# Kernel tuning notes

Hardware: AMD Instinct MI355X
Metric: run time of the kernel (lower is better)

Reference implementation:

```python
import jax, jax.numpy as jnp
import numpy as np

# dims: batch, seq, d_model, d_hidden, routed experts, top-k, shared experts
B, S, D, H, E_R, K, E_S = 2, 1024, 1024, 512, 64, 6, 2
EPS = 1.1920929e-07  # torch.finfo(float32).eps, RMSNorm default when eps=None


def setup_inputs() -> dict:
    key = jax.random.key(0)
    ks = jax.random.split(key, 8)
    u = lambda k, shape, b: jax.random.uniform(k, shape, jnp.float32, -b, b)
    bd = 1.0 / np.sqrt(D)   # bound for W1 (1/sqrt(d_input)) and W2 (1/sqrt(d_output)=1/sqrt(D))
    bh = 1.0 / np.sqrt(H)
    return {
        "x": jax.random.normal(ks[0], (B, S, D), jnp.float32),
        "norm_w": jnp.ones((D,), jnp.float32),            # RMSNorm weight
        "Wr": u(ks[1], (E_R, D), bd),                      # router Linear weight (no bias)
        "sW1": u(ks[2], (E_S, D, H), bd), "sb1": jnp.zeros((E_S, 1, H), jnp.float32),
        "sW2": u(ks[3], (E_S, H, D), bd), "sb2": jnp.zeros((E_S, 1, D), jnp.float32),
        "sWg": u(ks[4], (H, H), bh),                       # shared-experts SwiGLU gate weight
        "rW1": u(ks[5], (E_R, D, H), bd), "rb1": jnp.zeros((E_R, 1, H), jnp.float32),
        "rW2": u(ks[6], (E_R, H, D), bd), "rb2": jnp.zeros((E_R, 1, D), jnp.float32),
        "rWg": u(ks[7], (H, H), bh),                       # routed-experts SwiGLU gate weight
        "bias": jnp.full((E_R,), 1.0 / E_R, jnp.float32), # routing bias buffer (expert_bias=True)
    }


def _rmsnorm(x, w):
    ms = jnp.mean(x * x, axis=-1, keepdims=True)
    return x * jax.lax.rsqrt(ms + EPS) * w


def _swiglu(h, Wg):
    # SwiGLU(d_model=H): silu(h @ Wg) * h, elementwise gate over hidden dim
    return jax.nn.silu(h @ Wg) * h


def reference(x, norm_w, Wr, sW1, sb1, sW2, sb2, sWg, rW1, rb1, rW2, rb2, rWg, bias):
    xn = _rmsnorm(x, norm_w)
    t = xn.reshape(-1, D)                                  # (T, D) tokens
    # --- shared experts, summed over expert axis ---
    hs = jnp.einsum('td,edh->teh', t, sW1) + sb1[None, :, 0, :]
    hs = _swiglu(hs, sWg)
    shared = jnp.einsum('teh,ehd->td', hs, sW2) + jnp.sum(sb2[:, 0, :], axis=0)
    # --- router ---
    raw = t @ Wr.T                                         # (T, E_R) raw affinity
    aff = jax.lax.stop_gradient(raw) + bias                # detached + bias for top-k selection
    _, idx = jax.lax.top_k(aff, K)                         # (T, K)
    # --- routed experts: dense all-expert FFN, gather top-k outputs ---
    # (mathematically identical to the source's per-token weight gather,
    #  but avoids materializing (T,K,D,H) weight tensors)
    h = jnp.einsum('td,edh->teh', t, rW1) + rb1[None, :, 0, :]   # (T, E_R, H)
    h = _swiglu(h, rWg)
    out_all = jnp.einsum('teh,ehd->ted', h, rW2) + rb2[None, :, 0, :]  # (T, E_R, D)
    out_k = jnp.take_along_axis(out_all, idx[:, :, None], axis=1)      # (T, K, D)
    aff_k = jnp.take_along_axis(raw, idx, axis=1)                      # (T, K) raw (undetached)
    w = aff_k / jnp.sum(aff_k, axis=-1, keepdims=True)                 # expert_bias=True path
    routed = jnp.einsum('tk,tkd->td', w, out_k)                        # (T, D)
    return x + (shared + routed).reshape(B, S, D)
```

## Files before the change

### kernel.cpp

```cpp
#include <hip/hip_runtime.h>
#include <cstdint>
#include <cstddef>

typedef unsigned short u16;
typedef unsigned int u32;
typedef __attribute__((ext_vector_type(8))) short bh8;
typedef __attribute__((ext_vector_type(4))) float fx4;

#define T_TOK 2048
#define D_DIM 1024
#define H_DIM 512
#define N_EXP 64
#define K_TOP 6
#define N_ASG (T_TOK * K_TOP)

__device__ __forceinline__ float bf2f(u16 v) {
    union { u32 u; float f; } c; c.u = ((u32)v) << 16; return c.f;
}
__device__ __forceinline__ u16 f2bf(float f) {
    union { u32 u; float f; } c; c.f = f;
    u32 u = c.u;
    return (u16)((u + 0x7fffu + ((u >> 16) & 1u)) >> 16);
}

__global__ __launch_bounds__(256) void routernorm_k(
    const float* __restrict__ x, const float* __restrict__ nw,
    const float* __restrict__ Wr, float* __restrict__ raw, u16* __restrict__ xnb)
{
    int t = blockIdx.x, tid = threadIdx.x;
    __shared__ float xs[D_DIM];
    __shared__ float ps[256];
    __shared__ float red[4];
    int d0 = tid << 2;
    float4 xv = *(const float4*)(x + (size_t)t * D_DIM + d0);
    float ss = xv.x * xv.x + xv.y * xv.y + xv.z * xv.z + xv.w * xv.w;
    #pragma unroll
    for (int o = 32; o > 0; o >>= 1) ss += __shfl_down(ss, o);
    if ((tid & 63) == 0) red[tid >> 6] = ss;
    __syncthreads();
    float ms = (red[0] + red[1] + red[2] + red[3]) * (1.f / (float)D_DIM);
    float sc = rsqrtf(ms + 1.1920929e-07f);
    float4 wv = *(const float4*)(nw + d0);
    float4 xf;
    xf.x = xv.x * sc * wv.x;
    xf.y = xv.y * sc * wv.y;
    xf.z = xv.z * sc * wv.z;
    xf.w = xv.w * sc * wv.w;
    *(float4*)&xs[d0] = xf;
    ushort4 ob;
    ob.x = f2bf(xf.x); ob.y = f2bf(xf.y); ob.z = f2bf(xf.z); ob.w = f2bf(xf.w);
    *(ushort4*)(xnb + (size_t)t * D_DIM + d0) = ob;
    __syncthreads();
    int e = tid & 63, part = tid >> 6;
    const float* wr = Wr + (size_t)e * D_DIM + part * 256;
    const float* xp = &xs[part * 256];
    float s = 0.f;
    #pragma unroll 8
    for (int i = 0; i < 256; i += 4) {
        float4 w4 = *(const float4*)(wr + i);
        s += xp[i] * w4.x + xp[i + 1] * w4.y + xp[i + 2] * w4.z + xp[i + 3] * w4.w;
    }
    ps[tid] = s;
    __syncthreads();
    if (part == 0) raw[(size_t)t * N_EXP + e] = ps[e] + ps[64 + e] + ps[128 + e] + ps[192 + e];
}

__global__ void topk_k(const float* __restrict__ raw, const float* __restrict__ ebias,
                       int* __restrict__ cnt, int* __restrict__ tki, float* __restrict__ tkw)
{
    int t = blockIdx.x, lane = threadIdx.x;
    float r = raw[(size_t)t * N_EXP + lane];
    float cur = r + ebias[lane];
    int selI[K_TOP]; float selR[K_TOP];
    #pragma unroll
    for (int k = 0; k < K_TOP; ++k) {
        float v = cur; int id = lane;
        #pragma unroll
        for (int o = 32; o > 0; o >>= 1) {
            float v2 = __shfl_down(v, o); int i2 = __shfl_down(id, o);
            if (v2 > v || (v2 == v && i2 < id)) { v = v2; id = i2; }
        }
        id = __shfl(id, 0);
        if (lane == id) cur = -3.4e38f;
        selI[k] = id;
        selR[k] = __shfl(r, id);
    }
    float s = 0.f;
    #pragma unroll
    for (int k = 0; k < K_TOP; ++k) s += selR[k];
    if (lane < K_TOP) {
        tki[t * K_TOP + lane] = selI[lane];
        tkw[t * K_TOP + lane] = selR[lane] / s;
        atomicAdd(&cnt[selI[lane]], 1);
    }
}

__global__ void scan_k(const int* __restrict__ cnt, int* __restrict__ offs, int* __restrict__ fill)
{
    int lane = threadIdx.x;
    int c = cnt[lane];
    int s = c;
    #pragma unroll
    for (int o = 1; o < 64; o <<= 1) {
        int v = __shfl_up(s, o);
        if (lane >= o) s += v;
    }
    int excl = s - c;
    offs[lane] = excl;
    fill[lane] = excl;
    if (lane == 63) offs[N_EXP] = s;
}

__global__ void fill_k(const int* __restrict__ tki, const float* __restrict__ tkw,
                       int* __restrict__ fill, int* __restrict__ atok, float* __restrict__ aw)
{
    int t = blockIdx.x, lane = threadIdx.x;
    if (lane < K_TOP) {
        int e = tki[t * K_TOP + lane];
        int p = atomicAdd(&fill[e], 1);
        atok[p] = t;
        aw[p] = tkw[t * K_TOP + lane];
    }
}

__global__ __launch_bounds__(256) void convAll_k(
    const float* __restrict__ rW1, const float* __restrict__ sW1,
    const float* __restrict__ rW2, const float* __restrict__ sW2,
    const float* __restrict__ rWg, const float* __restrict__ sWg,
    u16* __restrict__ W1f, u16* __restrict__ W2f, u16* __restrict__ Wgf)
{
    int id = blockIdx.x;
    const float* src; u16* dst;
    int K, N, n0, k0;
    const size_t MS = (size_t)H_DIM * D_DIM;
    if (id < 66 * 128) {
        int mat = id >> 7, tile = id & 127;
        K = D_DIM; N = H_DIM;
        src = (mat < N_EXP ? rW1 + (size_t)mat * MS : sW1 + (size_t)(mat - N_EXP) * MS);
        dst = W1f + (size_t)mat * MS;
        n0 = (tile & 7) << 6; k0 = (tile >> 3) << 6;
    } else if (id < 2 * 66 * 128) {
        id -= 66 * 128;
        int mat = id >> 7, tile = id & 127;
        K = H_DIM; N = D_DIM;
        src = (mat < N_EXP ? rW2 + (size_t)mat * MS : sW2 + (size_t)(mat - N_EXP) * MS);
        dst = W2f + (size_t)mat * MS;
        n0 = (tile & 15) << 6; k0 = (tile >> 4) << 6;
    } else {
        id -= 2 * 66 * 128;
        int mat = id >> 6, tile = id & 63;
        K = H_DIM; N = H_DIM;
        src = (mat == 0 ? rWg : sWg);
        dst = Wgf + (size_t)mat * (H_DIM * H_DIM);
        n0 = (tile & 7) << 6; k0 = (tile >> 3) << 6;
    }

    __shared__ u16 t[64][72];
    int tid = threadIdx.x;
    int kr = tid >> 4, c4 = (tid & 15) << 2;
    #pragma unroll
    for (int rr = 0; rr < 4; ++rr) {
        int k = (rr << 4) + kr;
        float4 v = *(const float4*)(src + (size_t)(k0 + k) * N + n0 + c4);
        t[c4 + 0][k] = f2bf(v.x);
        t[c4 + 1][k] = f2bf(v.y);
        t[c4 + 2][k] = f2bf(v.z);
        t[c4 + 3][k] = f2bf(v.w);
    }
    __syncthreads();
    int lane = tid & 63, g = tid >> 6;
    int nr = lane & 15, kq = lane >> 4;
    #pragma unroll
    for (int f = 0; f < 2; ++f) {
        int fragId = g + (f << 2);
        int ntile = fragId >> 1, kb = fragId & 1;
        bh8 v = *(const bh8*)&t[(ntile << 4) + nr][(kb << 5) + (kq << 3)];
        size_t fi = (((size_t)((n0 >> 4) + ntile) * (size_t)(K >> 5)
                      + (size_t)((k0 >> 5) + kb)) << 9) + (size_t)(lane << 3);
        *(bh8*)(dst + fi) = v;
    }
}

__global__ __launch_bounds__(256, 2) void moe_ffn6_k(
    const u16* __restrict__ xnb,
    const u16* __restrict__ W1f,
    const u16* __restrict__ Wgf,
    const u16* __restrict__ W2f,
    const float* __restrict__ rb1, const float* __restrict__ rb2,
    const float* __restrict__ sb1, const float* __restrict__ sb2,
    const int* __restrict__ offs, const int* __restrict__ atok,
    const float* __restrict__ aw, float* __restrict__ accG)
{
    int id = blockIdx.x;
    int xcd = id & 7, rest = id >> 3, grp = rest >> 6, slab = rest & 63;
    int e, rowBase, end;
    bool routed;
    if (grp < 8) {
        e = (grp << 3) + xcd;
        routed = true;
        rowBase = offs[e] + (slab << 5);
        end = offs[e + 1];
    } else {
        int f = (slab << 3) + xcd;
        if (f >= 128) return;
        e = N_EXP + (f & 1);
        routed = false;
        rowBase = (f >> 1) << 5;
        end = T_TOK;
    }
    if (rowBase >= end) return;
    int rows = end - rowBase; if (rows > 32) rows = 32;

    __shared__ int   tok[32];
    __shared__ float wt[32];
    __shared__ u16 hA[32 * 520];

    int tid = threadIdx.x;
    if (tid < 32) {
        int cl = rowBase + tid; if (cl >= end) cl = end - 1;
        tok[tid] = routed ? atok[cl] : cl;
        wt[tid]  = routed ? aw[cl] : 1.0f;
    }
    __syncthreads();

    int w = tid >> 6, lane = tid & 63, quad = lane >> 4, l15 = lane & 15;
    int n0w = w << 7;

    const u16* W1e = W1f + (size_t)e * (H_DIM * D_DIM);
    const u16* W2e = W2f + (size_t)e * (H_DIM * D_DIM);
    const u16* Wge = Wgf + (routed ? 0 : (size_t)(H_DIM * H_DIM));
    const float* b1 = routed ? rb1 + e * H_DIM : sb1 + (e - N_EXP) * H_DIM;
    const float* b2 = routed ? rb2 + e * D_DIM : sb2 + (e - N_EXP) * D_DIM;

    {
        const u16* a0p = xnb + (size_t)tok[l15] * D_DIM + (quad << 3);
        const u16* a1p = xnb + (size_t)tok[16 + l15] * D_DIM + (quad << 3);
        const u16* bp  = W1e + ((size_t)w << 17) + (lane << 3);
        fx4 ac0[8] = {}, ac1[8] = {};
        bh8 bA[8], bB[8], aA0, aA1, aB0, aB1;
        #pragma unroll
        for (int ct = 0; ct < 8; ++ct) bA[ct] = *(const bh8*)(bp + (ct << 14));
        aA0 = *(const bh8*)a0p;
        aA1 = *(const bh8*)a1p;
        #pragma unroll 1
        for (int kbi = 0; kbi < 32; kbi += 2) {
            #pragma unroll
            for (int ct = 0; ct < 8; ++ct) bB[ct] = *(const bh8*)(bp + (((ct << 5) + kbi + 1) << 9));
            aB0 = *(const bh8*)(a0p + ((kbi + 1) << 5));
            aB1 = *(const bh8*)(a1p + ((kbi + 1) << 5));
            #pragma unroll
            for (int ct = 0; ct < 8; ++ct) {
                ac0[ct] = __builtin_amdgcn_mfma_f32_16x16x32_bf16(aA0, bA[ct], ac0[ct], 0, 0, 0);
                ac1[ct] = __builtin_amdgcn_mfma_f32_16x16x32_bf16(aA1, bA[ct], ac1[ct], 0, 0, 0);
            }
            #pragma unroll
            for (int ct = 0; ct < 8; ++ct) bA[ct] = *(const bh8*)(bp + (((ct << 5) + kbi + 2) << 9));
            aA0 = *(const bh8*)(a0p + ((kbi + 2) << 5));
            aA1 = *(const bh8*)(a1p + ((kbi + 2) << 5));
            #pragma unroll
            for (int ct = 0; ct < 8; ++ct) {
                ac0[ct] = __builtin_amdgcn_mfma_f32_16x16x32_bf16(aB0, bB[ct], ac0[ct], 0, 0, 0);
                ac1[ct] = __builtin_amdgcn_mfma_f32_16x16x32_bf16(aB1, bB[ct], ac1[ct], 0, 0, 0);
            }
        }
        #pragma unroll
        for (int ct = 0; ct < 8; ++ct) {
            int col = n0w + (ct << 4) + l15;
            float bv = b1[col];
            #pragma unroll
            for (int r = 0; r < 4; ++r) {
                int r0 = (quad << 2) + r;
                hA[r0 * 520 + col]        = f2bf(ac0[ct][r] + bv);
                hA[(16 + r0) * 520 + col] = f2bf(ac1[ct][r] + bv);
            }
        }
    }
    __syncthreads();

    {
        const u16* A0 = hA + l15 * 520 + (quad << 3);
        const u16* A1 = hA + (16 + l15) * 520 + (quad << 3);
        const u16* bp = Wge + ((size_t)w << 16) + (lane << 3);
        fx4 ac0[8] = {}, ac1[8] = {};
        bh8 bA[8], bB[8], aA0, aA1, aB0, aB1;
        #pragma unroll
        for (int ct = 0; ct < 8; ++ct) bA[ct] = *(const bh8*)(bp + (ct << 13));
        aA0 = *(const bh8*)A0;
        aA1 = *(const bh8*)A1;
        #pragma unroll 1
        for (int kbi = 0; kbi < 16; kbi += 2) {
            #pragma unroll
            for (int ct = 0; ct < 8; ++ct) bB[ct] = *(const bh8*)(bp + (((ct << 4) + kbi + 1) << 9));
            aB0 = *(const bh8*)(A0 + ((kbi + 1) << 5));
            aB1 = *(const bh8*)(A1 + ((kbi + 1) << 5));
            #pragma unroll
            for (int ct = 0; ct < 8; ++ct) {
                ac0[ct] = __builtin_amdgcn_mfma_f32_16x16x32_bf16(aA0, bA[ct], ac0[ct], 0, 0, 0);
                ac1[ct] = __builtin_amdgcn_mfma_f32_16x16x32_bf16(aA1, bA[ct], ac1[ct], 0, 0, 0);
            }
            #pragma unroll
            for (int ct = 0; ct < 8; ++ct) bA[ct] = *(const bh8*)(bp + (((ct << 4) + kbi + 2) << 9));
            aA0 = *(const bh8*)(A0 + ((kbi + 2) << 5));
            aA1 = *(const bh8*)(A1 + ((kbi + 2) << 5));
            #pragma unroll
            for (int ct = 0; ct < 8; ++ct) {
                ac0[ct] = __builtin_amdgcn_mfma_f32_16x16x32_bf16(aB0, bB[ct], ac0[ct], 0, 0, 0);
                ac1[ct] = __builtin_amdgcn_mfma_f32_16x16x32_bf16(aB1, bB[ct], ac1[ct], 0, 0, 0);
            }
        }
        __syncthreads();
        #pragma unroll
        for (int ct = 0; ct < 8; ++ct) {
            int col = n0w + (ct << 4) + l15;
            #pragma unroll
            for (int r = 0; r < 4; ++r) {
                int r0 = (quad << 2) + r;
                float g0 = ac0[ct][r];
                float h0 = bf2f(hA[r0 * 520 + col]);
                hA[r0 * 520 + col] = f2bf(h0 * g0 * (1.f / (1.f + __expf(-g0))));
                int r1 = 16 + r0;
                float g1 = ac1[ct][r];
                float h1 = bf2f(hA[r1 * 520 + col]);
                hA[r1 * 520 + col] = f2bf(h1 * g1 * (1.f / (1.f + __expf(-g1))));
            }
        }
    }
    __syncthreads();

    #pragma unroll 1
    for (int half = 0; half < 2; ++half) {
        int n0 = (w << 8) + (half << 7);
        const u16* A0 = hA + l15 * 520 + (quad << 3);
        const u16* A1 = hA + (16 + l15) * 520 + (quad << 3);
        const u16* bp = W2e + (((size_t)((w << 4) + (half << 3))) << 13) + (lane << 3);
        fx4 ac0[8] = {}, ac1[8] = {};
        bh8 bA[8], bB[8], aA0, aA1, aB0, aB1;
        #pragma unroll
        for (int ct = 0; ct < 8; ++ct) bA[ct] = *(const bh8*)(bp + (ct << 13));
        aA0 = *(const bh8*)A0;
        aA1 = *(const bh8*)A1;
        #pragma unroll 1
        for (int kbi = 0; kbi < 16; kbi += 2) {
            #pragma unroll
            for (int ct = 0; ct < 8; ++ct) bB[ct] = *(const bh8*)(bp + (((ct << 4) + kbi + 1) << 9));
            aB0 = *(const bh8*)(A0 + ((kbi + 1) << 5));
            aB1 = *(const bh8*)(A1 + ((kbi + 1) << 5));
            #pragma unroll
            for (int ct = 0; ct < 8; ++ct) {
                ac0[ct] = __builtin_amdgcn_mfma_f32_16x16x32_bf16(aA0, bA[ct], ac0[ct], 0, 0, 0);
                ac1[ct] = __builtin_amdgcn_mfma_f32_16x16x32_bf16(aA1, bA[ct], ac1[ct], 0, 0, 0);
            }
            #pragma unroll
            for (int ct = 0; ct < 8; ++ct) bA[ct] = *(const bh8*)(bp + (((ct << 4) + kbi + 2) << 9));
            aA0 = *(const bh8*)(A0 + ((kbi + 2) << 5));
            aA1 = *(const bh8*)(A1 + ((kbi + 2) << 5));
            #pragma unroll
            for (int ct = 0; ct < 8; ++ct) {
                ac0[ct] = __builtin_amdgcn_mfma_f32_16x16x32_bf16(aB0, bB[ct], ac0[ct], 0, 0, 0);
                ac1[ct] = __builtin_amdgcn_mfma_f32_16x16x32_bf16(aB1, bB[ct], ac1[ct], 0, 0, 0);
            }
        }
        #pragma unroll
        for (int ct = 0; ct < 8; ++ct) {
            int col = n0 + (ct << 4) + l15;
            float bv = b2[col];
            #pragma unroll
            for (int r = 0; r < 4; ++r) {
                int r0 = (quad << 2) + r;
                if (r0 < rows)
                    atomicAdd(&accG[(size_t)tok[r0] * D_DIM + col], wt[r0] * (ac0[ct][r] + bv));
                int r1 = 16 + r0;
                if (r1 < rows)
                    atomicAdd(&accG[(size_t)tok[r1] * D_DIM + col], wt[r1] * (ac1[ct][r] + bv));
            }
        }
    }
}

template<int ROUTED>
__global__ __launch_bounds__(256) void moe_ffn_k(
    const u16* __restrict__ xnb,
    const float* __restrict__ W1b, const float* __restrict__ Wg,
    const float* __restrict__ W2b,
    const float* __restrict__ b1b, const float* __restrict__ b2b,
    const int* __restrict__ offs, const int* __restrict__ atok,
    const float* __restrict__ aw, float* __restrict__ accG)
{
    int e = blockIdx.z;
    int start = ROUTED ? offs[e] : 0;
    int end   = ROUTED ? offs[e + 1] : T_TOK;
    int rowBase = start + (blockIdx.y << 5);
    if (rowBase >= end) return;
    int rows = end - rowBase; if (rows > 32) rows = 32;

    __shared__ int   tok[32];
    __shared__ float wt[32];
    __shared__ u16 hA[32 * 520];
    __shared__ u16 hG[32 * 520];
    __shared__ u16 As[32 * 32];
    __shared__ u16 Bs[64 * 36];

    int tid = threadIdx.x;
    if (tid < 32) {
        int cl = rowBase + tid; if (cl >= end) cl = end - 1;
        tok[tid] = ROUTED ? atok[cl] : cl;
        wt[tid]  = ROUTED ? aw[cl] : 1.0f;
    }
    __syncthreads();

    const float* W1 = W1b + (size_t)e * (D_DIM * H_DIM);
    const float* W2 = W2b + (size_t)e * (D_DIM * H_DIM);
    const float* b1 = b1b + e * H_DIM;
    const float* b2 = b2b + e * D_DIM;

    int w = tid >> 6, lane = tid & 63, quad = lane >> 4, l15 = lane & 15;
    int sr2 = tid >> 3, sc2 = (tid & 7) << 2;

    for (int nc = 0; nc < 8; ++nc) {
        int n0 = nc << 6;
        fx4 a0 = {}; fx4 a1 = {};
        for (int kc = 0; kc < 32; ++kc) {
            int kb = kc << 5;
            int2 av = *(const int2*)(xnb + (size_t)tok[sr2] * D_DIM + kb + sc2);
            const float* cp = W1 + n0 + lane;
            int kx = kb + (w << 3);
            u32 p[4];
            #pragma unroll
            for (int jj = 0; jj < 4; ++jj) {
                u32 lo = f2bf(cp[(size_t)(kx + 2 * jj) * H_DIM]);
                u32 hi = f2bf(cp[(size_t)(kx + 2 * jj + 1) * H_DIM]);
                p[jj] = lo | (hi << 16);
            }
            __syncthreads();
            *(int2*)&As[sr2 * 32 + sc2] = av;
            u16* bsw = &Bs[lane * 36 + (w << 3)];
            uint2 q0; q0.x = p[0]; q0.y = p[1];
            uint2 q1; q1.x = p[2]; q1.y = p[3];
            *(uint2*)bsw = q0;
            *(uint2*)(bsw + 4) = q1;
            __syncthreads();
            bh8 af0 = *(const bh8*)&As[l15 * 32 + (quad << 3)];
            bh8 af1 = *(const bh8*)&As[(16 + l15) * 32 + (quad << 3)];
            const u16* brp = &Bs[((w << 4) + l15) * 36 + (quad << 3)];
            union { bh8 v; uint2 u2[2]; } bf;
            bf.u2[0] = *(const uint2*)brp;
            bf.u2[1] = *(const uint2*)(brp + 4);
            a0 = __builtin_amdgcn_mfma_f32_16x16x32_bf16(af0, bf.v, a0, 0, 0, 0);
            a1 = __builtin_amdgcn_mfma_f32_16x16x32_bf16(af1, bf.v, a1, 0, 0, 0);
        }
        int col = n0 + (w << 4) + l15;
        float bv = b1[col];
        #pragma unroll
        for (int r = 0; r < 4; ++r) {
            hA[((quad << 2) + r) * 520 + col]      = f2bf(a0[r] + bv);
            hA[(16 + (quad << 2) + r) * 520 + col] = f2bf(a1[r] + bv);
        }
    }
    __syncthreads();

    for (int nc = 0; nc < 8; ++nc) {
        int n0 = nc << 6;
        fx4 a0 = {}; fx4 a1 = {};
        for (int kc = 0; kc < 16; ++kc) {
            int kb = kc << 5;
            const float* cp = Wg + n0 + lane;
            int kx = kb + (w << 3);
            u32 p[4];
            #pragma unroll
            for (int jj = 0; jj < 4; ++jj) {
                u32 lo = f2bf(cp[(size_t)(kx + 2 * jj) * H_DIM]);
                u32 hi = f2bf(cp[(size_t)(kx + 2 * jj + 1) * H_DIM]);
                p[jj] = lo | (hi << 16);
            }
            __syncthreads();
            u16* bsw = &Bs[lane * 36 + (w << 3)];
            uint2 q0; q0.x = p[0]; q0.y = p[1];
            uint2 q1; q1.x = p[2]; q1.y = p[3];
            *(uint2*)bsw = q0;
            *(uint2*)(bsw + 4) = q1;
            __syncthreads();
            bh8 af0 = *(const bh8*)&hA[l15 * 520 + kb + (quad << 3)];
            bh8 af1 = *(const bh8*)&hA[(16 + l15) * 520 + kb + (quad << 3)];
            const u16* brp = &Bs[((w << 4) + l15) * 36 + (quad << 3)];
            union { bh8 v; uint2 u2[2]; } bf;
            bf.u2[0] = *(const uint2*)brp;
            bf.u2[1] = *(const uint2*)(brp + 4);
            a0 = __builtin_amdgcn_mfma_f32_16x16x32_bf16(af0, bf.v, a0, 0, 0, 0);
            a1 = __builtin_amdgcn_mfma_f32_16x16x32_bf16(af1, bf.v, a1, 0, 0, 0);
        }
        int col = n0 + (w << 4) + l15;
        #pragma unroll
        for (int r = 0; r < 4; ++r) {
            int r0 = (quad << 2) + r;
            float h0 = bf2f(hA[r0 * 520 + col]);
            float g0 = a0[r];
            hG[r0 * 520 + col] = f2bf(h0 * g0 * (1.f / (1.f + __expf(-g0))));
            int r1 = 16 + r0;
            float h1 = bf2f(hA[r1 * 520 + col]);
            float g1 = a1[r];
            hG[r1 * 520 + col] = f2bf(h1 * g1 * (1.f / (1.f + __expf(-g1))));
        }
    }
    __syncthreads();

    for (int nc = 0; nc < 16; ++nc) {
        int n0 = nc << 6;
        fx4 a0 = {}; fx4 a1 = {};
        for (int kc = 0; kc < 16; ++kc) {
            int kb = kc << 5;
            const float* cp = W2 + n0 + lane;
            int kx = kb + (w << 3);
            u32 p[4];
            #pragma unroll
            for (int jj = 0; jj < 4; ++jj) {
                u32 lo = f2bf(cp[(size_t)(kx + 2 * jj) * D_DIM]);
                u32 hi = f2bf(cp[(size_t)(kx + 2 * jj + 1) * D_DIM]);
                p[jj] = lo | (hi << 16);
            }
            __syncthreads();
            u16* bsw = &Bs[lane * 36 + (w << 3)];
            uint2 q0; q0.x = p[0]; q0.y = p[1];
            uint2 q1; q1.x = p[2]; q1.y = p[3];
            *(uint2*)bsw = q0;
            *(uint2*)(bsw + 4) = q1;
            __syncthreads();
            bh8 af0 = *(const bh8*)&hG[l15 * 520 + kb + (quad << 3)];
            bh8 af1 = *(const bh8*)&hG[(16 + l15) * 520 + kb + (quad << 3)];
            const u16* brp = &Bs[((w << 4) + l15) * 36 + (quad << 3)];
            union { bh8 v; uint2 u2[2]; } bf;
            bf.u2[0] = *(const uint2*)brp;
            bf.u2[1] = *(const uint2*)(brp + 4);
            a0 = __builtin_amdgcn_mfma_f32_16x16x32_bf16(af0, bf.v, a0, 0, 0, 0);
            a1 = __builtin_amdgcn_mfma_f32_16x16x32_bf16(af1, bf.v, a1, 0, 0, 0);
        }
        int col = n0 + (w << 4) + l15;
        float bv = b2[col];
        #pragma unroll
        for (int r = 0; r < 4; ++r) {
            int lr0 = (quad << 2) + r;
            if (lr0 < rows)
                atomicAdd(&accG[(size_t)tok[lr0] * D_DIM + col], wt[lr0] * (a0[r] + bv));
            int lr1 = 16 + lr0;
            if (lr1 < rows)
                atomicAdd(&accG[(size_t)tok[lr1] * D_DIM + col], wt[lr1] * (a1[r] + bv));
        }
    }
}

__global__ __launch_bounds__(256) void final_k(
    const float* __restrict__ x, const float* __restrict__ acc, float* __restrict__ out)
{
    size_t i = ((size_t)blockIdx.x * 256 + threadIdx.x) << 2;
    float4 xv = *(const float4*)(x + i);
    float4 a = *(const float4*)(acc + i);
    float4 o;
    o.x = xv.x + a.x;
    o.y = xv.y + a.y;
    o.z = xv.z + a.z;
    o.w = xv.w + a.w;
    *(float4*)(out + i) = o;
}

extern "C" void kernel_launch(void* const* d_in, const int* in_sizes, int n_in,
                              void* d_out, int out_size, void* d_ws, size_t ws_size,
                              hipStream_t stream)
{
    const float* x     = (const float*)d_in[0];
    const float* nw    = (const float*)d_in[1];
    const float* Wr    = (const float*)d_in[2];
    const float* sW1   = (const float*)d_in[3];
    const float* sb1   = (const float*)d_in[4];
    const float* sW2   = (const float*)d_in[5];
    const float* sb2   = (const float*)d_in[6];
    const float* sWg   = (const float*)d_in[7];
    const float* rW1   = (const float*)d_in[8];
    const float* rb1   = (const float*)d_in[9];
    const float* rW2   = (const float*)d_in[10];
    const float* rb2   = (const float*)d_in[11];
    const float* rWg   = (const float*)d_in[12];
    const float* ebias = (const float*)d_in[13];
    float* out = (float*)d_out;
    (void)in_sizes; (void)n_in; (void)out_size;

    char* wp = (char*)d_ws;
    auto alloc = [&](size_t b) { char* p = wp; wp += (b + 255) & ~(size_t)255; return p; };
    int*   cnt  = (int*)alloc(N_EXP * 4);
    int*   offs = (int*)alloc((N_EXP + 1) * 4);
    int*   fill = (int*)alloc(N_EXP * 4);
    int*   tki  = (int*)alloc((size_t)T_TOK * K_TOP * 4);
    float* tkw  = (float*)alloc((size_t)T_TOK * K_TOP * 4);
    int*   atok = (int*)alloc((size_t)N_ASG * 4);
    float* aw   = (float*)alloc((size_t)N_ASG * 4);
    float* raw  = (float*)alloc((size_t)T_TOK * N_EXP * 4);
    u16*   xnb  = (u16*)alloc((size_t)T_TOK * D_DIM * 2);
    float* acc  = (float*)alloc((size_t)T_TOK * D_DIM * 4);
    u16* W1f = (u16*)alloc((size_t)(N_EXP + 2) * H_DIM * D_DIM * 2);
    u16* W2f = (u16*)alloc((size_t)(N_EXP + 2) * H_DIM * D_DIM * 2);
    u16* Wgf = (u16*)alloc((size_t)2 * H_DIM * H_DIM * 2);
    alloc(1 << 16);
    bool fast = (size_t)(wp - (char*)d_ws) <= ws_size;

    hipMemsetAsync(cnt, 0, N_EXP * 4, stream);
    hipMemsetAsync(acc, 0, (size_t)T_TOK * D_DIM * 4, stream);

    dim3 b256(256);
    routernorm_k<<<T_TOK, b256, 0, stream>>>(x, nw, Wr, raw, xnb);
    topk_k<<<T_TOK, dim3(64), 0, stream>>>(raw, ebias, cnt, tki, tkw);
    scan_k<<<1, dim3(64), 0, stream>>>(cnt, offs, fill);
    fill_k<<<T_TOK, dim3(64), 0, stream>>>(tki, tkw, fill, atok, aw);

    if (fast) {
        convAll_k<<<dim3(2 * 66 * 128 + 2 * 64), b256, 0, stream>>>(
            rW1, sW1, rW2, sW2, rWg, sWg, W1f, W2f, Wgf);

        moe_ffn6_k<<<dim3(8 * 9 * 64), b256, 0, stream>>>(
            xnb, W1f, Wgf, W2f, rb1, rb2, sb1, sb2, offs, atok, aw, acc);
    } else {
        moe_ffn_k<1><<<dim3(1, 64, N_EXP), b256, 0, stream>>>(
            xnb, rW1, rWg, rW2, rb1, rb2, offs, atok, aw, acc);
        moe_ffn_k<0><<<dim3(1, 64, 2), b256, 0, stream>>>(
            xnb, sW1, sWg, sW2, sb1, sb2, offs, atok, aw, acc);
    }

    final_k<<<(T_TOK * D_DIM) / 1024, b256, 0, stream>>>(x, acc, out);
}
```

Baseline: 716.6 us.

## Split fused expert FFN into three GEMM kernels and batch router-norm tokens

The single fused expert kernel, which computed W1, the SwiGLU gate and W2 per 32-row slab using shared memory, is replaced by three separate kernels. They exchange intermediate hidden activations through global bf16 buffers, and each kernel splits the output columns over an extra grid dimension. This gives many more, lighter blocks with higher occupancy hints, aiming to improve latency hiding and load balance. The cost is extra global memory traffic for the intermediate buffers and two more launches. The router/RMSNorm kernel also now handles 4 tokens per block, so each router weight load is reused across those tokens.

```diff
diff --git a/kernel.cpp b/kernel.cpp
--- a/kernel.cpp
+++ b/kernel.cpp
@@ -13,6 +13,8 @@
 #define N_EXP 64
 #define K_TOP 6
 #define N_ASG (T_TOK * K_TOP)
+#define R_TOT (N_ASG + 2 * T_TOK)
+#define GRID_E (8 * 9 * 64)
 
 __device__ __forceinline__ float bf2f(u16 v) {
     union { u32 u; float f; } c; c.u = ((u32)v) << 16; return c.f;
@@ -23,46 +25,65 @@
     return (u16)((u + 0x7fffu + ((u >> 16) & 1u)) >> 16);
 }
 
-__global__ __launch_bounds__(256) void routernorm_k(
+__global__ __launch_bounds__(256) void rn4_k(
     const float* __restrict__ x, const float* __restrict__ nw,
     const float* __restrict__ Wr, float* __restrict__ raw, u16* __restrict__ xnb)
 {
-    int t = blockIdx.x, tid = threadIdx.x;
-    __shared__ float xs[D_DIM];
-    __shared__ float ps[256];
-    __shared__ float red[4];
+    int t0 = blockIdx.x << 2, tid = threadIdx.x;
+    __shared__ float xs[4][D_DIM];
+    __shared__ float ps[4][256];
+    __shared__ float red4[4][4];
     int d0 = tid << 2;
-    float4 xv = *(const float4*)(x + (size_t)t * D_DIM + d0);
-    float ss = xv.x * xv.x + xv.y * xv.y + xv.z * xv.z + xv.w * xv.w;
-    #pragma unroll
-    for (int o = 32; o > 0; o >>= 1) ss += __shfl_down(ss, o);
-    if ((tid & 63) == 0) red[tid >> 6] = ss;
-    __syncthreads();
-    float ms = (red[0] + red[1] + red[2] + red[3]) * (1.f / (float)D_DIM);
-    float sc = rsqrtf(ms + 1.1920929e-07f);
     float4 wv = *(const float4*)(nw + d0);
-    float4 xf;
-    xf.x = xv.x * sc * wv.x;
-    xf.y = xv.y * sc * wv.y;
-    xf.z = xv.z * sc * wv.z;
-    xf.w = xv.w * sc * wv.w;
-    *(float4*)&xs[d0] = xf;
-    ushort4 ob;
-    ob.x = f2bf(xf.x); ob.y = f2bf(xf.y); ob.z = f2bf(xf.z); ob.w = f2bf(xf.w);
-    *(ushort4*)(xnb + (size_t)t * D_DIM + d0) = ob;
+    float4 xv[4];
+    #pragma unroll
+    for (int tt = 0; tt < 4; ++tt) {
+        xv[tt] = *(const float4*)(x + (size_t)(t0 + tt) * D_DIM + d0);
+        float ss = xv[tt].x * xv[tt].x + xv[tt].y * xv[tt].y
+                 + xv[tt].z * xv[tt].z + xv[tt].w * xv[tt].w;
+        #pragma unroll
+        for (int o = 32; o > 0; o >>= 1) ss += __shfl_down(ss, o);
+        if ((tid & 63) == 0) red4[tt][tid >> 6] = ss;
+    }
+    __syncthreads();
+    #pragma unroll
+    for (int tt = 0; tt < 4; ++tt) {
+        float ms = (red4[tt][0] + red4[tt][1] + red4[tt][2] + red4[tt][3]) * (1.f / (float)D_DIM);
+        float sc = rsqrtf(ms + 1.1920929e-07f);
+        float4 xf;
+        xf.x = xv[tt].x * sc * wv.x;
+        xf.y = xv[tt].y * sc * wv.y;
+        xf.z = xv[tt].z * sc * wv.z;
+        xf.w = xv[tt].w * sc * wv.w;
+        *(float4*)&xs[tt][d0] = xf;
+        ushort4 ob;
+        ob.x = f2bf(xf.x); ob.y = f2bf(xf.y); ob.z = f2bf(xf.z); ob.w = f2bf(xf.w);
+        *(ushort4*)(xnb + (size_t)(t0 + tt) * D_DIM + d0) = ob;
+    }
     __syncthreads();
     int e = tid & 63, part = tid >> 6;
     const float* wr = Wr + (size_t)e * D_DIM + part * 256;
-    const float* xp = &xs[part * 256];
-    float s = 0.f;
-    #pragma unroll 8
+    float s0 = 0.f, s1 = 0.f, s2 = 0.f, s3 = 0.f;
+    const float* xp0 = &xs[0][part * 256];
+    const float* xp1 = &xs[1][part * 256];
+    const float* xp2 = &xs[2][part * 256];
+    const float* xp3 = &xs[3][part * 256];
+    #pragma unroll 4
     for (int i = 0; i < 256; i += 4) {
         float4 w4 = *(const float4*)(wr + i);
-        s += xp[i] * w4.x + xp[i + 1] * w4.y + xp[i + 2] * w4.z + xp[i + 3] * w4.w;
-    }
-    ps[tid] = s;
-    __syncthreads();
-    if (part == 0) raw[(size_t)t * N_EXP + e] = ps[e] + ps[64 + e] + ps[128 + e] + ps[192 + e];
+        s0 += xp0[i] * w4.x + xp0[i+1] * w4.y + xp0[i+2] * w4.z + xp0[i+3] * w4.w;
+        s1 += xp1[i] * w4.x + xp1[i+1] * w4.y + xp1[i+2] * w4.z + xp1[i+3] * w4.w;
+        s2 += xp2[i] * w4.x + xp2[i+1] * w4.y + xp2[i+2] * w4.z + xp2[i+3] * w4.w;
+        s3 += xp3[i] * w4.x + xp3[i+1] * w4.y + xp3[i+2] * w4.z + xp3[i+3] * w4.w;
+    }
+    ps[0][tid] = s0; ps[1][tid] = s1; ps[2][tid] = s2; ps[3][tid] = s3;
+    __syncthreads();
+    if (part == 0) {
+        #pragma unroll
+        for (int tt = 0; tt < 4; ++tt)
+            raw[(size_t)(t0 + tt) * N_EXP + e] =
+                ps[tt][e] + ps[tt][64 + e] + ps[tt][128 + e] + ps[tt][192 + e];
+    }
 }
 
 __global__ void topk_k(const float* __restrict__ raw, const float* __restrict__ ebias,
@@ -181,198 +202,218 @@
     }
 }
 
-__global__ __launch_bounds__(256, 2) void moe_ffn6_k(
-    const u16* __restrict__ xnb,
-    const u16* __restrict__ W1f,
-    const u16* __restrict__ Wgf,
-    const u16* __restrict__ W2f,
-    const float* __restrict__ rb1, const float* __restrict__ rb2,
-    const float* __restrict__ sb1, const float* __restrict__ sb2,
+__device__ __forceinline__ bool slabDecode(
+    int bx, const int* __restrict__ offs,
+    int& e, int& rowBase, int& rows, int& tokBase)
+{
+    int xcd = bx & 7, rest = bx >> 3, grp = rest >> 6, slab = rest & 63;
+    if (grp < 8) {
+        e = (grp << 3) + xcd;
+        int s0 = offs[e], s1 = offs[e + 1];
+        rowBase = s0 + (slab << 5);
+        if (rowBase >= s1) return false;
+        rows = s1 - rowBase; if (rows > 32) rows = 32;
+        tokBase = -1;
+        return true;
+    }
+    int f = (slab << 3) + xcd;
+    if (f >= 128) return false;
+    int sh = f & 1;
+    e = N_EXP + sh;
+    tokBase = (f >> 1) << 5;
+    rowBase = N_ASG + (sh << 11) + tokBase;
+    rows = 32;
+    return true;
+}
+
+__global__ __launch_bounds__(256, 4) void p1_k(
+    const u16* __restrict__ xnb, const u16* __restrict__ W1f,
+    const float* __restrict__ rb1, const float* __restrict__ sb1,
+    const int* __restrict__ offs, const int* __restrict__ atok,
+    u16* __restrict__ h)
+{
+    int e, rowBase, rows, tokBase;
+    if (!slabDecode(blockIdx.x, offs, e, rowBase, rows, tokBase)) return;
+
+    __shared__ int tok[32];
+    int tid = threadIdx.x;
+    if (tid < 32) {
+        int cl = tid < rows ? tid : rows - 1;
+        tok[tid] = (tokBase < 0) ? atok[rowBase + cl] : tokBase + tid;
+    }
+    __syncthreads();
+
+    int w = tid >> 6, lane = tid & 63, quad = lane >> 4, l15 = lane & 15;
+    int cg = blockIdx.y;
+    int nt0 = (cg << 4) + (w << 2);
+    const u16* bp = W1f + (size_t)e * (H_DIM * D_DIM)
+                  + (((size_t)nt0 << 5) << 9) + (lane << 3);
+    const u16* a0p = xnb + (size_t)tok[l15] * D_DIM + (quad << 3);
+    const u16* a1p = xnb + (size_t)tok[16 + l15] * D_DIM + (quad << 3);
+    const float* b1 = (tokBase < 0) ? rb1 + e * H_DIM : sb1 + (e - N_EXP) * H_DIM;
+
+    fx4 ac0[4] = {}, ac1[4] = {};
+    bh8 bA[4], bB[4], aA0, aA1, aB0, aB1;
+    #pragma unroll
+    for (int ct = 0; ct < 4; ++ct) bA[ct] = *(const bh8*)(bp + ((size_t)(ct << 5) << 9));
+    aA0 = *(const bh8*)a0p; aA1 = *(const bh8*)a1p;
+    #pragma unroll 1
+    for (int kb = 0; kb < 32; kb += 2) {
+        #pragma unroll
+        for (int ct = 0; ct < 4; ++ct) bB[ct] = *(const bh8*)(bp + (((ct << 5) + kb + 1) << 9));
+        aB0 = *(const bh8*)(a0p + ((kb + 1) << 5));
+        aB1 = *(const bh8*)(a1p + ((kb + 1) << 5));
+        #pragma unroll
+        for (int ct = 0; ct < 4; ++ct) {
+            ac0[ct] = __builtin_amdgcn_mfma_f32_16x16x32_bf16(aA0, bA[ct], ac0[ct], 0, 0, 0);
+            ac1[ct] = __builtin_amdgcn_mfma_f32_16x16x32_bf16(aA1, bA[ct], ac1[ct], 0, 0, 0);
+        }
+        #pragma unroll
+        for (int ct = 0; ct < 4; ++ct) bA[ct] = *(const bh8*)(bp + (((ct << 5) + kb + 2) << 9));
+        aA0 = *(const bh8*)(a0p + ((kb + 2) << 5));
+        aA1 = *(const bh8*)(a1p + ((kb + 2) << 5));
+        #pragma unroll
+        for (int ct = 0; ct < 4; ++ct) {
+            ac0[ct] = __builtin_amdgcn_mfma_f32_16x16x32_bf16(aB0, bB[ct], ac0[ct], 0, 0, 0);
+            ac1[ct] = __builtin_amdgcn_mfma_f32_16x16x32_bf16(aB1, bB[ct], ac1[ct], 0, 0, 0);
+        }
+    }
+    #pragma unroll
+    for (int ct = 0; ct < 4; ++ct) {
+        int col = ((nt0 + ct) << 4) + l15;
+        float bv = b1[col];
+        #pragma unroll
+        for (int r = 0; r < 4; ++r) {
+            int r0 = (quad << 2) + r;
+            if (r0 < rows) h[(size_t)(rowBase + r0) * H_DIM + col] = f2bf(ac0[ct][r] + bv);
+            int r1 = 16 + r0;
+            if (r1 < rows) h[(size_t)(rowBase + r1) * H_DIM + col] = f2bf(ac1[ct][r] + bv);
+        }
+    }
+}
+
+__global__ __launch_bounds__(256, 4) void p2_k(
+    const u16* __restrict__ hbuf, const u16* __restrict__ Wgf, u16* __restrict__ hg)
+{
+    int rowBase = blockIdx.x << 5;
+    int tid = threadIdx.x;
+    int w = tid >> 6, lane = tid & 63, quad = lane >> 4, l15 = lane & 15;
+    int cg = blockIdx.y;
+    int nt0 = (cg << 4) + (w << 2);
+    const u16* bp = Wgf + (rowBase < N_ASG ? 0 : (size_t)(H_DIM * H_DIM))
+                  + (((size_t)nt0 << 4) << 9) + (lane << 3);
+    const u16* a0p = hbuf + (size_t)(rowBase + l15) * H_DIM + (quad << 3);
+    const u16* a1p = hbuf + (size_t)(rowBase + 16 + l15) * H_DIM + (quad << 3);
+
+    fx4 ac0[4] = {}, ac1[4] = {};
+    bh8 bA[4], bB[4], aA0, aA1, aB0, aB1;
+    #pragma unroll
+    for (int ct = 0; ct < 4; ++ct) bA[ct] = *(const bh8*)(bp + ((size_t)(ct << 4) << 9));
+    aA0 = *(const bh8*)a0p; aA1 = *(const bh8*)a1p;
+    #pragma unroll 1
+    for (int kb = 0; kb < 16; kb += 2) {
+        #pragma unroll
+        for (int ct = 0; ct < 4; ++ct) bB[ct] = *(const bh8*)(bp + (((ct << 4) + kb + 1) << 9));
+        aB0 = *(const bh8*)(a0p + ((kb + 1) << 5));
+        aB1 = *(const bh8*)(a1p + ((kb + 1) << 5));
+        #pragma unroll
+        for (int ct = 0; ct < 4; ++ct) {
+            ac0[ct] = __builtin_amdgcn_mfma_f32_16x16x32_bf16(aA0, bA[ct], ac0[ct], 0, 0, 0);
+            ac1[ct] = __builtin_amdgcn_mfma_f32_16x16x32_bf16(aA1, bA[ct], ac1[ct], 0, 0, 0);
+        }
+        #pragma unroll
+        for (int ct = 0; ct < 4; ++ct) bA[ct] = *(const bh8*)(bp + (((ct << 4) + kb + 2) << 9));
+        aA0 = *(const bh8*)(a0p + ((kb + 2) << 5));
+        aA1 = *(const bh8*)(a1p + ((kb + 2) << 5));
+        #pragma unroll
+        for (int ct = 0; ct < 4; ++ct) {
+            ac0[ct] = __builtin_amdgcn_mfma_f32_16x16x32_bf16(aB0, bB[ct], ac0[ct], 0, 0, 0);
+            ac1[ct] = __builtin_amdgcn_mfma_f32_16x16x32_bf16(aB1, bB[ct], ac1[ct], 0, 0, 0);
+        }
+    }
+    #pragma unroll
+    for (int ct = 0; ct < 4; ++ct) {
+        int col = ((nt0 + ct) << 4) + l15;
+        #pragma unroll
+        for (int r = 0; r < 4; ++r) {
+            int r0 = (quad << 2) + r;
+            size_t i0 = (size_t)(rowBase + r0) * H_DIM + col;
+            float g0 = ac0[ct][r], h0 = bf2f(hbuf[i0]);
+            hg[i0] = f2bf(h0 * g0 * (1.f / (1.f + __expf(-g0))));
+            int r1 = 16 + r0;
+            size_t i1 = (size_t)(rowBase + r1) * H_DIM + col;
+            float g1 = ac1[ct][r], h1 = bf2f(hbuf[i1]);
+            hg[i1] = f2bf(h1 * g1 * (1.f / (1.f + __expf(-g1))));
+        }
+    }
+}
+
+__global__ __launch_bounds__(256, 4) void p3_k(
+    const u16* __restrict__ hg, const u16* __restrict__ W2f,
+    const float* __restrict__ rb2, const float* __restrict__ sb2,
     const int* __restrict__ offs, const int* __restrict__ atok,
     const float* __restrict__ aw, float* __restrict__ accG)
 {
-    int id = blockIdx.x;
-    int xcd = id & 7, rest = id >> 3, grp = rest >> 6, slab = rest & 63;
-    int e, rowBase, end;
-    bool routed;
-    if (grp < 8) {
-        e = (grp << 3) + xcd;
-        routed = true;
-        rowBase = offs[e] + (slab << 5);
-        end = offs[e + 1];
-    } else {
-        int f = (slab << 3) + xcd;
-        if (f >= 128) return;
-        e = N_EXP + (f & 1);
-        routed = false;
-        rowBase = (f >> 1) << 5;
-        end = T_TOK;
-    }
-    if (rowBase >= end) return;
-    int rows = end - rowBase; if (rows > 32) rows = 32;
-
-    __shared__ int   tok[32];
+    int e, rowBase, rows, tokBase;
+    if (!slabDecode(blockIdx.x, offs, e, rowBase, rows, tokBase)) return;
+
+    __shared__ int tok[32];
     __shared__ float wt[32];
-    __shared__ u16 hA[32 * 520];
-
     int tid = threadIdx.x;
     if (tid < 32) {
-        int cl = rowBase + tid; if (cl >= end) cl = end - 1;
-        tok[tid] = routed ? atok[cl] : cl;
-        wt[tid]  = routed ? aw[cl] : 1.0f;
+        int cl = tid < rows ? tid : rows - 1;
+        if (tokBase < 0) { tok[tid] = atok[rowBase + cl]; wt[tid] = aw[rowBase + cl]; }
+        else             { tok[tid] = tokBase + tid;      wt[tid] = 1.0f; }
     }
     __syncthreads();
 
     int w = tid >> 6, lane = tid & 63, quad = lane >> 4, l15 = lane & 15;
-    int n0w = w << 7;
-
-    const u16* W1e = W1f + (size_t)e * (H_DIM * D_DIM);
-    const u16* W2e = W2f + (size_t)e * (H_DIM * D_DIM);
-    const u16* Wge = Wgf + (routed ? 0 : (size_t)(H_DIM * H_DIM));
-    const float* b1 = routed ? rb1 + e * H_DIM : sb1 + (e - N_EXP) * H_DIM;
-    const float* b2 = routed ? rb2 + e * D_DIM : sb2 + (e - N_EXP) * D_DIM;
-
-    {
-        const u16* a0p = xnb + (size_t)tok[l15] * D_DIM + (quad << 3);
-        const u16* a1p = xnb + (size_t)tok[16 + l15] * D_DIM + (quad << 3);
-        const u16* bp  = W1e + ((size_t)w << 17) + (lane << 3);
-        fx4 ac0[8] = {}, ac1[8] = {};
-        bh8 bA[8], bB[8], aA0, aA1, aB0, aB1;
-        #pragma unroll
-        for (int ct = 0; ct < 8; ++ct) bA[ct] = *(const bh8*)(bp + (ct << 14));
-        aA0 = *(const bh8*)a0p;
-        aA1 = *(const bh8*)a1p;
-        #pragma unroll 1
-        for (int kbi = 0; kbi < 32; kbi += 2) {
-            #pragma unroll
-            for (int ct = 0; ct < 8; ++ct) bB[ct] = *(const bh8*)(bp + (((ct << 5) + kbi + 1) << 9));
-            aB0 = *(const bh8*)(a0p + ((kbi + 1) << 5));
-            aB1 = *(const bh8*)(a1p + ((kbi + 1) << 5));
-            #pragma unroll
-            for (int ct = 0; ct < 8; ++ct) {
-                ac0[ct] = __builtin_amdgcn_mfma_f32_16x16x32_bf16(aA0, bA[ct], ac0[ct], 0, 0, 0);
-                ac1[ct] = __builtin_amdgcn_mfma_f32_16x16x32_bf16(aA1, bA[ct], ac1[ct], 0, 0, 0);
-            }
-            #pragma unroll
-            for (int ct = 0; ct < 8; ++ct) bA[ct] = *(const bh8*)(bp + (((ct << 5) + kbi + 2) << 9));
-            aA0 = *(const bh8*)(a0p + ((kbi + 2) << 5));
-            aA1 = *(const bh8*)(a1p + ((kbi + 2) << 5));
-            #pragma unroll
-            for (int ct = 0; ct < 8; ++ct) {
-                ac0[ct] = __builtin_amdgcn_mfma_f32_16x16x32_bf16(aB0, bB[ct], ac0[ct], 0, 0, 0);
-                ac1[ct] = __builtin_amdgcn_mfma_f32_16x16x32_bf16(aB1, bB[ct], ac1[ct], 0, 0, 0);
-            }
-        }
-        #pragma unroll
-        for (int ct = 0; ct < 8; ++ct) {
-            int col = n0w + (ct << 4) + l15;
-            float bv = b1[col];
-            #pragma unroll
-            for (int r = 0; r < 4; ++r) {
-                int r0 = (quad << 2) + r;
-                hA[r0 * 520 + col]        = f2bf(ac0[ct][r] + bv);
-                hA[(16 + r0) * 520 + col] = f2bf(ac1[ct][r] + bv);
-            }
-        }
-    }
-    __syncthreads();
-
-    {
-        const u16* A0 = hA + l15 * 520 + (quad << 3);
-        const u16* A1 = hA + (16 + l15) * 520 + (quad << 3);
-        const u16* bp = Wge + ((size_t)w << 16) + (lane << 3);
-        fx4 ac0[8] = {}, ac1[8] = {};
-        bh8 bA[8], bB[8], aA0, aA1, aB0, aB1;
-        #pragma unroll
-        for (int ct = 0; ct < 8; ++ct) bA[ct] = *(const bh8*)(bp + (ct << 13));
-        aA0 = *(const bh8*)A0;
-        aA1 = *(const bh8*)A1;
-        #pragma unroll 1
-        for (int kbi = 0; kbi < 16; kbi += 2) {
-            #pragma unroll
-            for (int ct = 0; ct < 8; ++ct) bB[ct] = *(const bh8*)(bp + (((ct << 4) + kbi + 1) << 9));
-            aB0 = *(const bh8*)(A0 + ((kbi + 1) << 5));
-            aB1 = *(const bh8*)(A1 + ((kbi + 1) << 5));
-            #pragma unroll
-            for (int ct = 0; ct < 8; ++ct) {
-                ac0[ct] = __builtin_amdgcn_mfma_f32_16x16x32_bf16(aA0, bA[ct], ac0[ct], 0, 0, 0);
-                ac1[ct] = __builtin_amdgcn_mfma_f32_16x16x32_bf16(aA1, bA[ct], ac1[ct], 0, 0, 0);
-            }
-            #pragma unroll
-            for (int ct = 0; ct < 8; ++ct) bA[ct] = *(const bh8*)(bp + (((ct << 4) + kbi + 2) << 9));
-            aA0 = *(const bh8*)(A0 + ((kbi + 2) << 5));
-            aA1 = *(const bh8*)(A1 + ((kbi + 2) << 5));
-            #pragma unroll
-            for (int ct = 0; ct < 8; ++ct) {
-                ac0[ct] = __builtin_amdgcn_mfma_f32_16x16x32_bf16(aB0, bB[ct], ac0[ct], 0, 0, 0);
-                ac1[ct] = __builtin_amdgcn_mfma_f32_16x16x32_bf16(aB1, bB[ct], ac1[ct], 0, 0, 0);
-            }
-        }
-        __syncthreads();
-        #pragma unroll
-        for (int ct = 0; ct < 8; ++ct) {
-            int col = n0w + (ct << 4) + l15;
-            #pragma unroll
-            for (int r = 0; r < 4; ++r) {
-                int r0 = (quad << 2) + r;
-                float g0 = ac0[ct][r];
-                float h0 = bf2f(hA[r0 * 520 + col]);
-                hA[r0 * 520 + col] = f2bf(h0 * g0 * (1.f / (1.f + __expf(-g0))));
-                int r1 = 16 + r0;
-                float g1 = ac1[ct][r];
-                float h1 = bf2f(hA[r1 * 520 + col]);
-                hA[r1 * 520 + col] = f2bf(h1 * g1 * (1.f / (1.f + __expf(-g1))));
-            }
-        }
-    }
-    __syncthreads();
-
+    int cg = blockIdx.y;
+    int nt0 = (cg << 4) + (w << 2);
+    const u16* bp = W2f + (size_t)e * (H_DIM * D_DIM)
+                  + (((size_t)nt0 << 4) << 9) + (lane << 3);
+    const u16* a0p = hg + (size_t)(rowBase + l15) * H_DIM + (quad << 3);
+    const u16* a1p = hg + (size_t)(rowBase + 16 + l15) * H_DIM + (quad << 3);
+    const float* b2 = (tokBase < 0) ? rb2 + e * D_DIM : sb2 + (e - N_EXP) * D_DIM;
+
+    fx4 ac0[4] = {}, ac1[4] = {};
+    bh8 bA[4], bB[4], aA0, aA1, aB0, aB1;
+    #pragma unroll
+    for (int ct = 0; ct < 4; ++ct) bA[ct] = *(const bh8*)(bp + ((size_t)(ct << 4) << 9));
+    aA0 = *(const bh8*)a0p; aA1 = *(const bh8*)a1p;
     #pragma unroll 1
-    for (int half = 0; half < 2; ++half) {
-        int n0 = (w << 8) + (half << 7);
-        const u16* A0 = hA + l15 * 520 + (quad << 3);
-        const u16* A1 = hA + (16 + l15) * 520 + (quad << 3);
-        const u16* bp = W2e + (((size_t)((w << 4) + (half << 3))) << 13) + (lane << 3);
-        fx4 ac0[8] = {}, ac1[8] = {};
-        bh8 bA[8], bB[8], aA0, aA1, aB0, aB1;
-        #pragma unroll
-        for (int ct = 0; ct < 8; ++ct) bA[ct] = *(const bh8*)(bp + (ct << 13));
-        aA0 = *(const bh8*)A0;
-        aA1 = *(const bh8*)A1;
-        #pragma unroll 1
-        for (int kbi = 0; kbi < 16; kbi += 2) {
-            #pragma unroll
-            for (int ct = 0; ct < 8; ++ct) bB[ct] = *(const bh8*)(bp + (((ct << 4) + kbi + 1) << 9));
-            aB0 = *(const bh8*)(A0 + ((kbi + 1) << 5));
-            aB1 = *(const bh8*)(A1 + ((kbi + 1) << 5));
-            #pragma unroll
-            for (int ct = 0; ct < 8; ++ct) {
-                ac0[ct] = __builtin_amdgcn_mfma_f32_16x16x32_bf16(aA0, bA[ct], ac0[ct], 0, 0, 0);
-                ac1[ct] = __builtin_amdgcn_mfma_f32_16x16x32_bf16(aA1, bA[ct], ac1[ct], 0, 0, 0);
-            }
-            #pragma unroll
-            for (int ct = 0; ct < 8; ++ct) bA[ct] = *(const bh8*)(bp + (((ct << 4) + kbi + 2) << 9));
-            aA0 = *(const bh8*)(A0 + ((kbi + 2) << 5));
-            aA1 = *(const bh8*)(A1 + ((kbi + 2) << 5));
-            #pragma unroll
-            for (int ct = 0; ct < 8; ++ct) {
-                ac0[ct] = __builtin_amdgcn_mfma_f32_16x16x32_bf16(aB0, bB[ct], ac0[ct], 0, 0, 0);
-                ac1[ct] = __builtin_amdgcn_mfma_f32_16x16x32_bf16(aB1, bB[ct], ac1[ct], 0, 0, 0);
-            }
-        }
-        #pragma unroll
-        for (int ct = 0; ct < 8; ++ct) {
-            int col = n0 + (ct << 4) + l15;
-            float bv = b2[col];
-            #pragma unroll
-            for (int r = 0; r < 4; ++r) {
-                int r0 = (quad << 2) + r;
-                if (r0 < rows)
-                    atomicAdd(&accG[(size_t)tok[r0] * D_DIM + col], wt[r0] * (ac0[ct][r] + bv));
-                int r1 = 16 + r0;
-                if (r1 < rows)
-                    atomicAdd(&accG[(size_t)tok[r1] * D_DIM + col], wt[r1] * (ac1[ct][r] + bv));
-            }
+    for (int kb = 0; kb < 16; kb += 2) {
+        #pragma unroll
+        for (int ct = 0; ct < 4; ++ct) bB[ct] = *(const bh8*)(bp + (((ct << 4) + kb + 1) << 9));
+        aB0 = *(const bh8*)(a0p + ((kb + 1) << 5));
+        aB1 = *(const bh8*)(a1p + ((kb + 1) << 5));
+        #pragma unroll
+        for (int ct = 0; ct < 4; ++ct) {
+            ac0[ct] = __builtin_amdgcn_mfma_f32_16x16x32_bf16(aA0, bA[ct], ac0[ct], 0, 0, 0);
+            ac1[ct] = __builtin_amdgcn_mfma_f32_16x16x32_bf16(aA1, bA[ct], ac1[ct], 0, 0, 0);
+        }
+        #pragma unroll
+        for (int ct = 0; ct < 4; ++ct) bA[ct] = *(const bh8*)(bp + (((ct << 4) + kb + 2) << 9));
+        aA0 = *(const bh8*)(a0p + ((kb + 2) << 5));
+        aA1 = *(const bh8*)(a1p + ((kb + 2) << 5));
+        #pragma unroll
+        for (int ct = 0; ct < 4; ++ct) {
+            ac0[ct] = __builtin_amdgcn_mfma_f32_16x16x32_bf16(aB0, bB[ct], ac0[ct], 0, 0, 0);
+            ac1[ct] = __builtin_amdgcn_mfma_f32_16x16x32_bf16(aB1, bB[ct], ac1[ct], 0, 0, 0);
+        }
+    }
+    #pragma unroll
+    for (int ct = 0; ct < 4; ++ct) {
+        int col = ((nt0 + ct) << 4) + l15;
+        float bv = b2[col];
+        #pragma unroll
+        for (int r = 0; r < 4; ++r) {
+            int r0 = (quad << 2) + r;
+            if (r0 < rows)
+                atomicAdd(&accG[(size_t)tok[r0] * D_DIM + col], wt[r0] * (ac0[ct][r] + bv));
+            int r1 = 16 + r0;
+            if (r1 < rows)
+                atomicAdd(&accG[(size_t)tok[r1] * D_DIM + col], wt[r1] * (ac1[ct][r] + bv));
         }
     }
 }
@@ -597,6 +638,8 @@
     u16* W1f = (u16*)alloc((size_t)(N_EXP + 2) * H_DIM * D_DIM * 2);
     u16* W2f = (u16*)alloc((size_t)(N_EXP + 2) * H_DIM * D_DIM * 2);
     u16* Wgf = (u16*)alloc((size_t)2 * H_DIM * H_DIM * 2);
+    u16* h   = (u16*)alloc((size_t)R_TOT * H_DIM * 2);
+    u16* hg  = (u16*)alloc((size_t)R_TOT * H_DIM * 2);
     alloc(1 << 16);
     bool fast = (size_t)(wp - (char*)d_ws) <= ws_size;
 
@@ -604,7 +647,7 @@
     hipMemsetAsync(acc, 0, (size_t)T_TOK * D_DIM * 4, stream);
 
     dim3 b256(256);
-    routernorm_k<<<T_TOK, b256, 0, stream>>>(x, nw, Wr, raw, xnb);
+    rn4_k<<<T_TOK / 4, b256, 0, stream>>>(x, nw, Wr, raw, xnb);
     topk_k<<<T_TOK, dim3(64), 0, stream>>>(raw, ebias, cnt, tki, tkw);
     scan_k<<<1, dim3(64), 0, stream>>>(cnt, offs, fill);
     fill_k<<<T_TOK, dim3(64), 0, stream>>>(tki, tkw, fill, atok, aw);
@@ -613,8 +656,9 @@
         convAll_k<<<dim3(2 * 66 * 128 + 2 * 64), b256, 0, stream>>>(
             rW1, sW1, rW2, sW2, rWg, sWg, W1f, W2f, Wgf);
 
-        moe_ffn6_k<<<dim3(8 * 9 * 64), b256, 0, stream>>>(
-            xnb, W1f, Wgf, W2f, rb1, rb2, sb1, sb2, offs, atok, aw, acc);
+        p1_k<<<dim3(GRID_E, 2), b256, 0, stream>>>(xnb, W1f, rb1, sb1, offs, atok, h);
+        p2_k<<<dim3(R_TOT / 32, 2), b256, 0, stream>>>(h, Wgf, hg);
+        p3_k<<<dim3(GRID_E, 4), b256, 0, stream>>>(hg, W2f, rb2, sb2, offs, atok, aw, acc);
     } else {
         moe_ffn_k<1><<<dim3(1, 64, N_EXP), b256, 0, stream>>>(
             xnb, rW1, rWg, rW2, rb1, rb2, offs, atok, aw, acc);
```

Result: faster. 651.6 us (-9.1%).
